# Kernel optimization log

Hardware: AMD Instinct MI355X
Metric: run time of the kernel (lower is better)

The kernel has to match this reference:

```python
import jax, jax.numpy as jnp
import numpy as np

NUM_TASKS, IN_SIZE, OUT_SIZE, N_ROWS = 64, 512, 512, 2048


def setup_inputs() -> dict:
    key = jax.random.key(0)
    k_x, k_t, k_w = jax.random.split(key, 3)
    inputs = jax.random.normal(k_x, (N_ROWS, IN_SIZE), dtype=jnp.float32)
    task_ids = jax.random.randint(k_t, (N_ROWS,), 0, NUM_TASKS, dtype=jnp.int64)
    # in_size == out_size path: identity + N(0, 0.03) perturbation per task
    W = (jnp.eye(IN_SIZE, OUT_SIZE, dtype=jnp.float32)[None]
         + 0.03 * jax.random.normal(k_w, (NUM_TASKS, IN_SIZE, OUT_SIZE), dtype=jnp.float32))
    return {"inputs": inputs, "task_ids": task_ids, "W": W}


def reference(inputs, task_ids, W):
    # Gather the full per-row weight matrix then batched vector-matrix multiply,
    # faithful to torch.einsum('ni,nio->no', inputs, W[task_ids]).
    aligned = W[task_ids]                       # [I, in, out]
    return jnp.einsum("ni,nio->no", inputs, aligned)  # [I, out]
```

## Files before the change

kernel.cpp:

```cpp
#include <hip/hip_runtime.h>


#define NDIM 512
#define KDIM 512
#define NCOL 32
#define KH   256

typedef _Float16 f16x8 __attribute__((ext_vector_type(8)));
typedef float    f32x4 __attribute__((ext_vector_type(4)));
typedef int      i32x4 __attribute__((ext_vector_type(4)));

__global__ __launch_bounds__(256, 4) void k_fused3(
    const float* __restrict__ x,
    const int*   __restrict__ tids,
    const float* __restrict__ W,
    float*       __restrict__ out,
    int n_rows)
{
    const int tid  = threadIdx.x;
    const int lane = tid & 63;
    const int wv   = tid >> 6;

    const int id    = blockIdx.x;
    const int task  = (id & 7) | ((id >> 7) << 3);
    const int c0    = ((id >> 3) & 15) * NCOL;

    __shared__ __align__(16) _Float16 Wt2[2][NCOL * KH];
    __shared__ unsigned short rlw[4 * 128];

    const int rbase = wv * 512 + lane * 8;
    int tval[8];
    if (rbase + 7 < n_rows) {
        const i32x4 a = *(const i32x4*)(tids + rbase);
        const i32x4 b = *(const i32x4*)(tids + rbase + 4);
        tval[0] = a[0]; tval[1] = a[1]; tval[2] = a[2]; tval[3] = a[3];
        tval[4] = b[0]; tval[5] = b[1]; tval[6] = b[2]; tval[7] = b[3];
    } else {
        #pragma unroll
        for (int j = 0; j < 8; ++j)
            tval[j] = (rbase + j < n_rows) ? tids[rbase + j] : -1;
    }

    const int sc4 = (tid & 7) * 4;
    const int ob  = tid >> 3;
    const float* Wg = W + (size_t)task * KDIM * NDIM + c0;
    float4 wr[8];
    #pragma unroll
    for (int j = 0; j < 8; ++j)
        wr[j] = *(const float4*)(Wg + (size_t)(ob * 8 + j) * NDIM + sc4);

    int cloc = 0;
    #pragma unroll
    for (int j = 0; j < 8; ++j) {
        const bool m = (tval[j] == task);
        const unsigned long long bal = __ballot(m);
        const int rank = __popcll(bal & ((1ull << lane) - 1ull));
        if (m) rlw[wv * 128 + cloc + rank] = (unsigned short)(rbase + j);
        cloc += __popcll(bal);
    }

    const int ml = lane & 15;
    const int q  = lane >> 4;

    auto load_half = [&](const float* xr, int t, f16x8* paf) {
        #pragma unroll
        for (int h = 0; h < 2; ++h) {
            f32x4 xa[8];
            #pragma unroll
            for (int k2 = 0; k2 < 4; ++k2) {
                const int ks = h * 4 + k2;
                xa[2 * k2]     = *(const f32x4*)(xr + t * KH + ks * 32 + q * 8);
                xa[2 * k2 + 1] = *(const f32x4*)(xr + t * KH + ks * 32 + q * 8 + 4);
            }
            #pragma unroll
            for (int k2 = 0; k2 < 4; ++k2) {
                f16x8 af;
                const float* a0 = (const float*)&xa[2 * k2];
                #pragma unroll
                for (int j = 0; j < 8; ++j) af[j] = (_Float16)a0[j];
                paf[h * 4 + k2] = af;
            }
        }
    };

    auto stage_half = [&](int t) {
        #pragma unroll
        for (int j2 = 0; j2 < 4; ++j2) {
            f16x8 h8;
            #pragma unroll
            for (int j = 0; j < 8; ++j)
                h8[j] = (_Float16)(((const float*)&wr[j])[j2]);
            const int c  = sc4 + j2;
            const int po = ob ^ (c & 7);
            *(f16x8*)&Wt2[t][c * KH + po * 8] = h8;
        }
    };

    auto mma_half = [&](int t, const f16x8* paf, f32x4* acc) {
        #pragma unroll
        for (int ks = 0; ks < 8; ++ks) {
            #pragma unroll
            for (int ct = 0; ct < 2; ++ct) {
                const int cB = ct * 16 + ml;
                const int po = (ks * 4 + q) ^ (cB & 7);
                const f16x8 bf = *(const f16x8*)&Wt2[t][cB * KH + po * 8];
                acc[ct] = __builtin_amdgcn_mfma_f32_16x16x32_f16(paf[ks], bf, acc[ct], 0, 0, 0);
            }
        }
    };

    auto store_rows = [&](int g0, const f32x4* acc) {
        #pragma unroll
        for (int rg = 0; rg < 4; ++rg) {
            const int pos = g0 + q * 4 + rg;
            if (pos < cloc) {
                float* op = out + (size_t)rlw[wv * 128 + pos] * NDIM + c0 + ml;
                op[0]  = acc[0][rg];
                op[16] = acc[1][rg];
            }
        }
    };

    const float* xr = x;
    f16x8 pafA[8];
    if (cloc > 0) {
        const int idx = (ml < cloc) ? ml : (cloc - 1);
        xr = x + (size_t)rlw[wv * 128 + idx] * KDIM;
        load_half(xr, 0, pafA);
    }

    stage_half(0);
    #pragma unroll
    for (int j = 0; j < 8; ++j)
        wr[j] = *(const float4*)(Wg + (size_t)(KH + ob * 8 + j) * NDIM + sc4);

    asm volatile("s_waitcnt lgkmcnt(0)" ::: "memory");
    __builtin_amdgcn_s_barrier();
    __builtin_amdgcn_sched_barrier(0);

    f32x4 acc[2] = {};
    if (cloc > 0) mma_half(0, pafA, acc);

    f16x8 pafB[8];
    if (cloc > 0) load_half(xr, 1, pafB);

    stage_half(1);

    asm volatile("s_waitcnt lgkmcnt(0)" ::: "memory");
    __builtin_amdgcn_s_barrier();
    __builtin_amdgcn_sched_barrier(0);

    if (cloc > 0) {
        mma_half(1, pafB, acc);
        store_rows(0, acc);
    }

    for (int g0 = 16; g0 < cloc; g0 += 16) {
        const int idx = g0 + ml;
        const float* xr2 = x + (size_t)rlw[wv * 128 + ((idx < cloc) ? idx : (cloc - 1))] * KDIM;
        f16x8 pf[8];
        f32x4 a2[2] = {};
        load_half(xr2, 0, pf);
        mma_half(0, pf, a2);
        load_half(xr2, 1, pf);
        mma_half(1, pf, a2);
        store_rows(g0, a2);
    }
}

extern "C" void kernel_launch(void* const* d_in, const int* in_sizes, int n_in,
                              void* d_out, int out_size, void* d_ws, size_t ws_size,
                              hipStream_t stream) {
    const float* x    = (const float*)d_in[0];
    const int*   tids = (const int*)d_in[1];
    const float* W    = (const float*)d_in[2];
    float*       out  = (float*)d_out;
    const int n_rows  = in_sizes[1];

    k_fused3<<<dim3(1024), dim3(256), 0, stream>>>(x, tids, W, out, n_rows);
}
```

Before: 107.3 us.

## Make blocks persistent over two work units and prefetch next unit's weights

The grid is halved and each block now processes two (task, column-slice) units in sequence. It reuses the loaded task ids and issues the next unit's first weight half while the current unit's MMAs and row tails run. This aims to hide global weight-load latency and amortize block launch and task-id loading. In exchange, per-block parallelism is lower, occupancy hints drop to 2 blocks per CU, and an extra barrier is added between units.

```diff
diff --git a/kernel.cpp b/kernel.cpp
--- a/kernel.cpp
+++ b/kernel.cpp
@@ -5,12 +5,14 @@
 #define KDIM 512
 #define NCOL 32
 #define KH   256
+#define GRID 512
+#define NUNIT 2
 
 typedef _Float16 f16x8 __attribute__((ext_vector_type(8)));
 typedef float    f32x4 __attribute__((ext_vector_type(4)));
 typedef int      i32x4 __attribute__((ext_vector_type(4)));
 
-__global__ __launch_bounds__(256, 4) void k_fused3(
+__global__ __launch_bounds__(256, 2) void k_fused4(
     const float* __restrict__ x,
     const int*   __restrict__ tids,
     const float* __restrict__ W,
@@ -20,12 +22,12 @@
     const int tid  = threadIdx.x;
     const int lane = tid & 63;
     const int wv   = tid >> 6;
-
-    const int id    = blockIdx.x;
-    const int task  = (id & 7) | ((id >> 7) << 3);
-    const int c0    = ((id >> 3) & 15) * NCOL;
-
-    __shared__ __align__(16) _Float16 Wt2[2][NCOL * KH];
+    const int ml   = lane & 15;
+    const int q    = lane >> 4;
+    const int sc4  = (tid & 7) * 4;
+    const int ob   = tid >> 3;
+
+    __shared__ __align__(16) _Float16 Wt[2][NCOL * KH];
     __shared__ unsigned short rlw[4 * 128];
 
     const int rbase = wv * 512 + lane * 8;
@@ -41,36 +43,39 @@
             tval[j] = (rbase + j < n_rows) ? tids[rbase + j] : -1;
     }
 
-    const int sc4 = (tid & 7) * 4;
-    const int ob  = tid >> 3;
-    const float* Wg = W + (size_t)task * KDIM * NDIM + c0;
+    int   cloc = 0;
+    int   c0   = 0;
+    const float* xr = x;
     float4 wr[8];
-    #pragma unroll
-    for (int j = 0; j < 8; ++j)
-        wr[j] = *(const float4*)(Wg + (size_t)(ob * 8 + j) * NDIM + sc4);
-
-    int cloc = 0;
-    #pragma unroll
-    for (int j = 0; j < 8; ++j) {
-        const bool m = (tval[j] == task);
-        const unsigned long long bal = __ballot(m);
-        const int rank = __popcll(bal & ((1ull << lane) - 1ull));
-        if (m) rlw[wv * 128 + cloc + rank] = (unsigned short)(rbase + j);
-        cloc += __popcll(bal);
-    }
-
-    const int ml = lane & 15;
-    const int q  = lane >> 4;
-
-    auto load_half = [&](const float* xr, int t, f16x8* paf) {
+
+    auto issueW = [&](const float* Wg, int h) {
+        #pragma unroll
+        for (int j = 0; j < 8; ++j)
+            wr[j] = *(const float4*)(Wg + (size_t)(h * KH + ob * 8 + j) * NDIM + sc4);
+    };
+
+    auto stageW = [&](int t) {
+        #pragma unroll
+        for (int j2 = 0; j2 < 4; ++j2) {
+            f16x8 h8;
+            #pragma unroll
+            for (int j = 0; j < 8; ++j)
+                h8[j] = (_Float16)(((const float*)&wr[j])[j2]);
+            const int c  = sc4 + j2;
+            const int po = ob ^ (c & 7);
+            *(f16x8*)&Wt[t][c * KH + po * 8] = h8;
+        }
+    };
+
+    auto load_half = [&](const float* xrp, int t, f16x8* paf) {
         #pragma unroll
         for (int h = 0; h < 2; ++h) {
             f32x4 xa[8];
             #pragma unroll
             for (int k2 = 0; k2 < 4; ++k2) {
                 const int ks = h * 4 + k2;
-                xa[2 * k2]     = *(const f32x4*)(xr + t * KH + ks * 32 + q * 8);
-                xa[2 * k2 + 1] = *(const f32x4*)(xr + t * KH + ks * 32 + q * 8 + 4);
+                xa[2 * k2]     = *(const f32x4*)(xrp + t * KH + ks * 32 + q * 8);
+                xa[2 * k2 + 1] = *(const f32x4*)(xrp + t * KH + ks * 32 + q * 8 + 4);
             }
             #pragma unroll
             for (int k2 = 0; k2 < 4; ++k2) {
@@ -83,19 +88,6 @@
         }
     };
 
-    auto stage_half = [&](int t) {
-        #pragma unroll
-        for (int j2 = 0; j2 < 4; ++j2) {
-            f16x8 h8;
-            #pragma unroll
-            for (int j = 0; j < 8; ++j)
-                h8[j] = (_Float16)(((const float*)&wr[j])[j2]);
-            const int c  = sc4 + j2;
-            const int po = ob ^ (c & 7);
-            *(f16x8*)&Wt2[t][c * KH + po * 8] = h8;
-        }
-    };
-
     auto mma_half = [&](int t, const f16x8* paf, f32x4* acc) {
         #pragma unroll
         for (int ks = 0; ks < 8; ++ks) {
@@ -103,7 +95,7 @@
             for (int ct = 0; ct < 2; ++ct) {
                 const int cB = ct * 16 + ml;
                 const int po = (ks * 4 + q) ^ (cB & 7);
-                const f16x8 bf = *(const f16x8*)&Wt2[t][cB * KH + po * 8];
+                const f16x8 bf = *(const f16x8*)&Wt[t][cB * KH + po * 8];
                 acc[ct] = __builtin_amdgcn_mfma_f32_16x16x32_f16(paf[ks], bf, acc[ct], 0, 0, 0);
             }
         }
@@ -121,50 +113,78 @@
         }
     };
 
-    const float* xr = x;
-    f16x8 pafA[8];
-    if (cloc > 0) {
-        const int idx = (ml < cloc) ? ml : (cloc - 1);
-        xr = x + (size_t)rlw[wv * 128 + idx] * KDIM;
-        load_half(xr, 0, pafA);
-    }
-
-    stage_half(0);
+    int task = (blockIdx.x & 7) | ((blockIdx.x >> 7) << 3);
+    c0 = ((blockIdx.x >> 3) & 15) * NCOL;
+    const float* Wg = W + (size_t)task * KDIM * NDIM + c0;
+    issueW(Wg, 0);
+
     #pragma unroll
-    for (int j = 0; j < 8; ++j)
-        wr[j] = *(const float4*)(Wg + (size_t)(KH + ob * 8 + j) * NDIM + sc4);
-
-    asm volatile("s_waitcnt lgkmcnt(0)" ::: "memory");
-    __builtin_amdgcn_s_barrier();
-    __builtin_amdgcn_sched_barrier(0);
-
-    f32x4 acc[2] = {};
-    if (cloc > 0) mma_half(0, pafA, acc);
-
-    f16x8 pafB[8];
-    if (cloc > 0) load_half(xr, 1, pafB);
-
-    stage_half(1);
-
-    asm volatile("s_waitcnt lgkmcnt(0)" ::: "memory");
-    __builtin_amdgcn_s_barrier();
-    __builtin_amdgcn_sched_barrier(0);
-
-    if (cloc > 0) {
-        mma_half(1, pafB, acc);
-        store_rows(0, acc);
-    }
-
-    for (int g0 = 16; g0 < cloc; g0 += 16) {
-        const int idx = g0 + ml;
-        const float* xr2 = x + (size_t)rlw[wv * 128 + ((idx < cloc) ? idx : (cloc - 1))] * KDIM;
-        f16x8 pf[8];
-        f32x4 a2[2] = {};
-        load_half(xr2, 0, pf);
-        mma_half(0, pf, a2);
-        load_half(xr2, 1, pf);
-        mma_half(1, pf, a2);
-        store_rows(g0, a2);
+    for (int uu = 0; uu < NUNIT; ++uu) {
+        cloc = 0;
+        #pragma unroll
+        for (int j = 0; j < 8; ++j) {
+            const bool m = (tval[j] == task);
+            const unsigned long long bal = __ballot(m);
+            const int rank = __popcll(bal & ((1ull << lane) - 1ull));
+            if (m) rlw[wv * 128 + cloc + rank] = (unsigned short)(rbase + j);
+            cloc += __popcll(bal);
+        }
+
+        f16x8 pafA[8], pafB[8];
+        if (cloc > 0) {
+            const int idx = (ml < cloc) ? ml : (cloc - 1);
+            xr = x + (size_t)rlw[wv * 128 + idx] * KDIM;
+            load_half(xr, 0, pafA);
+        }
+
+        stageW(0);
+        issueW(Wg, 1);
+        asm volatile("s_waitcnt lgkmcnt(0)" ::: "memory");
+        __builtin_amdgcn_s_barrier();
+        __builtin_amdgcn_sched_barrier(0);
+
+        f32x4 acc[2] = {};
+        if (cloc > 0) mma_half(0, pafA, acc);
+        if (cloc > 0) load_half(xr, 1, pafB);
+        stageW(1);
+
+        int ntask = 0, nc0 = 0;
+        const float* nWg = nullptr;
+        if (uu + 1 < NUNIT) {
+            const int nu = blockIdx.x + (uu + 1) * GRID;
+            ntask = (nu & 7) | ((nu >> 7) << 3);
+            nc0   = ((nu >> 3) & 15) * NCOL;
+            nWg   = W + (size_t)ntask * KDIM * NDIM + nc0;
+            issueW(nWg, 0);
+        }
+
+        asm volatile("s_waitcnt lgkmcnt(0)" ::: "memory");
+        __builtin_amdgcn_s_barrier();
+        __builtin_amdgcn_sched_barrier(0);
+
+        if (cloc > 0) {
+            mma_half(1, pafB, acc);
+            store_rows(0, acc);
+        }
+
+        for (int g0 = 16; g0 < cloc; g0 += 16) {
+            const int idx = g0 + ml;
+            const float* xr2 = x + (size_t)rlw[wv * 128 + ((idx < cloc) ? idx : (cloc - 1))] * KDIM;
+            f16x8 pf[8];
+            f32x4 a2[2] = {};
+            load_half(xr2, 0, pf);
+            mma_half(0, pf, a2);
+            load_half(xr2, 1, pf);
+            mma_half(1, pf, a2);
+            store_rows(g0, a2);
+        }
+
+        if (uu + 1 < NUNIT) {
+            asm volatile("s_waitcnt lgkmcnt(0)" ::: "memory");
+            __builtin_amdgcn_s_barrier();
+            __builtin_amdgcn_sched_barrier(0);
+            task = ntask; c0 = nc0; Wg = nWg;
+        }
     }
 }
 
@@ -177,5 +197,5 @@
     float*       out  = (float*)d_out;
     const int n_rows  = in_sizes[1];
 
-    k_fused3<<<dim3(1024), dim3(256), 0, stream>>>(x, tids, W, out, n_rows);
+    k_fused4<<<dim3(GRID), dim3(256), 0, stream>>>(x, tids, W, out, n_rows);
 }
```

Result: no change. 105.3 us (-1.8%).

## Widen per-block column tile to 64 and halve grid size

Applied to the files above, without the earlier changes.

Each block now covers 64 output columns instead of 32, so the grid drops from 1024 to 512 blocks. Every routed x row is loaded and converted to fp16 once per 64 columns rather than once per 32, which halves redundant x traffic and conversion work. W staging is split into two register batches with interleaved issue and stage steps to overlap the global loads. The costs are doubled LDS for the weight tile, more registers (launch bounds lowered to 2 blocks per CU), fewer blocks in flight, and a new clamp that caps each wave's row list at 128.

```diff
diff --git a/kernel.cpp b/kernel.cpp
--- a/kernel.cpp
+++ b/kernel.cpp
@@ -3,14 +3,15 @@
 
 #define NDIM 512
 #define KDIM 512
-#define NCOL 32
+#define NCOL 64
 #define KH   256
+#define GRID 512
 
 typedef _Float16 f16x8 __attribute__((ext_vector_type(8)));
 typedef float    f32x4 __attribute__((ext_vector_type(4)));
 typedef int      i32x4 __attribute__((ext_vector_type(4)));
 
-__global__ __launch_bounds__(256, 4) void k_fused3(
+__global__ __launch_bounds__(256, 2) void k_g64(
     const float* __restrict__ x,
     const int*   __restrict__ tids,
     const float* __restrict__ W,
@@ -20,13 +21,20 @@
     const int tid  = threadIdx.x;
     const int lane = tid & 63;
     const int wv   = tid >> 6;
+    const int ml   = lane & 15;
+    const int q    = lane >> 4;
+    const int cg   = tid & 15;
+    const int sc4  = cg * 4;
+    const int ot   = tid >> 4;
 
-    const int id    = blockIdx.x;
-    const int task  = (id & 7) | ((id >> 7) << 3);
-    const int c0    = ((id >> 3) & 15) * NCOL;
+    const int bid   = blockIdx.x;
+    const int task  = (bid & 7) | ((bid >> 6) << 3);
+    const int c0    = ((bid >> 3) & 7) * NCOL;
 
-    __shared__ __align__(16) _Float16 Wt2[2][NCOL * KH];
+    __shared__ __align__(16) _Float16 Wt[2][NCOL * KH];
     __shared__ unsigned short rlw[4 * 128];
+
+    const float* Wg = W + (size_t)task * KDIM * NDIM + c0;
 
     const int rbase = wv * 512 + lane * 8;
     int tval[8];
@@ -41,13 +49,30 @@
             tval[j] = (rbase + j < n_rows) ? tids[rbase + j] : -1;
     }
 
-    const int sc4 = (tid & 7) * 4;
-    const int ob  = tid >> 3;
-    const float* Wg = W + (size_t)task * KDIM * NDIM + c0;
-    float4 wr[8];
-    #pragma unroll
-    for (int j = 0; j < 8; ++j)
-        wr[j] = *(const float4*)(Wg + (size_t)(ob * 8 + j) * NDIM + sc4);
+    float4 wrA[8], wrB[8];
+
+    auto issueS = [&](int h, int s, float4 (&wb)[8]) {
+        const size_t kb = (size_t)(h * KH) + (size_t)(ot + 16 * s) * 8;
+        #pragma unroll
+        for (int j = 0; j < 8; ++j)
+            wb[j] = *(const float4*)(Wg + (kb + j) * NDIM + sc4);
+    };
+    auto stageS = [&](int h, int s, const float4 (&wb)[8]) {
+        const int oct = ot + 16 * s;
+        #pragma unroll
+        for (int j2 = 0; j2 < 4; ++j2) {
+            f16x8 h8;
+            #pragma unroll
+            for (int j = 0; j < 8; ++j)
+                h8[j] = (_Float16)(((const float*)&wb[j])[j2]);
+            const int c  = sc4 + j2;
+            const int po = oct ^ (c & 7);
+            *(f16x8*)&Wt[h][c * KH + po * 8] = h8;
+        }
+    };
+
+    issueS(0, 0, wrA);
+    issueS(0, 1, wrB);
 
     int cloc = 0;
     #pragma unroll
@@ -55,22 +80,21 @@
         const bool m = (tval[j] == task);
         const unsigned long long bal = __ballot(m);
         const int rank = __popcll(bal & ((1ull << lane) - 1ull));
-        if (m) rlw[wv * 128 + cloc + rank] = (unsigned short)(rbase + j);
+        const int slot = cloc + rank;
+        if (m && slot < 128) rlw[wv * 128 + slot] = (unsigned short)(rbase + j);
         cloc += __popcll(bal);
     }
+    if (cloc > 128) cloc = 128;
 
-    const int ml = lane & 15;
-    const int q  = lane >> 4;
-
-    auto load_half = [&](const float* xr, int t, f16x8* paf) {
+    auto load_half = [&](const float* xrp, int t, f16x8* paf) {
         #pragma unroll
         for (int h = 0; h < 2; ++h) {
             f32x4 xa[8];
             #pragma unroll
             for (int k2 = 0; k2 < 4; ++k2) {
                 const int ks = h * 4 + k2;
-                xa[2 * k2]     = *(const f32x4*)(xr + t * KH + ks * 32 + q * 8);
-                xa[2 * k2 + 1] = *(const f32x4*)(xr + t * KH + ks * 32 + q * 8 + 4);
+                xa[2 * k2]     = *(const f32x4*)(xrp + t * KH + ks * 32 + q * 8);
+                xa[2 * k2 + 1] = *(const f32x4*)(xrp + t * KH + ks * 32 + q * 8 + 4);
             }
             #pragma unroll
             for (int k2 = 0; k2 < 4; ++k2) {
@@ -83,27 +107,14 @@
         }
     };
 
-    auto stage_half = [&](int t) {
-        #pragma unroll
-        for (int j2 = 0; j2 < 4; ++j2) {
-            f16x8 h8;
-            #pragma unroll
-            for (int j = 0; j < 8; ++j)
-                h8[j] = (_Float16)(((const float*)&wr[j])[j2]);
-            const int c  = sc4 + j2;
-            const int po = ob ^ (c & 7);
-            *(f16x8*)&Wt2[t][c * KH + po * 8] = h8;
-        }
-    };
-
     auto mma_half = [&](int t, const f16x8* paf, f32x4* acc) {
         #pragma unroll
         for (int ks = 0; ks < 8; ++ks) {
             #pragma unroll
-            for (int ct = 0; ct < 2; ++ct) {
+            for (int ct = 0; ct < 4; ++ct) {
                 const int cB = ct * 16 + ml;
                 const int po = (ks * 4 + q) ^ (cB & 7);
-                const f16x8 bf = *(const f16x8*)&Wt2[t][cB * KH + po * 8];
+                const f16x8 bf = *(const f16x8*)&Wt[t][cB * KH + po * 8];
                 acc[ct] = __builtin_amdgcn_mfma_f32_16x16x32_f16(paf[ks], bf, acc[ct], 0, 0, 0);
             }
         }
@@ -117,34 +128,35 @@
                 float* op = out + (size_t)rlw[wv * 128 + pos] * NDIM + c0 + ml;
                 op[0]  = acc[0][rg];
                 op[16] = acc[1][rg];
+                op[32] = acc[2][rg];
+                op[48] = acc[3][rg];
             }
         }
     };
 
     const float* xr = x;
-    f16x8 pafA[8];
+    f16x8 pafA[8], pafB[8];
     if (cloc > 0) {
         const int idx = (ml < cloc) ? ml : (cloc - 1);
         xr = x + (size_t)rlw[wv * 128 + idx] * KDIM;
         load_half(xr, 0, pafA);
     }
 
-    stage_half(0);
-    #pragma unroll
-    for (int j = 0; j < 8; ++j)
-        wr[j] = *(const float4*)(Wg + (size_t)(KH + ob * 8 + j) * NDIM + sc4);
+    stageS(0, 0, wrA);
+    issueS(1, 0, wrA);
+    stageS(0, 1, wrB);
+    issueS(1, 1, wrB);
 
     asm volatile("s_waitcnt lgkmcnt(0)" ::: "memory");
     __builtin_amdgcn_s_barrier();
     __builtin_amdgcn_sched_barrier(0);
 
-    f32x4 acc[2] = {};
+    f32x4 acc[4] = {};
     if (cloc > 0) mma_half(0, pafA, acc);
-
-    f16x8 pafB[8];
     if (cloc > 0) load_half(xr, 1, pafB);
 
-    stage_half(1);
+    stageS(1, 0, wrA);
+    stageS(1, 1, wrB);
 
     asm volatile("s_waitcnt lgkmcnt(0)" ::: "memory");
     __builtin_amdgcn_s_barrier();
@@ -159,7 +171,7 @@
         const int idx = g0 + ml;
         const float* xr2 = x + (size_t)rlw[wv * 128 + ((idx < cloc) ? idx : (cloc - 1))] * KDIM;
         f16x8 pf[8];
-        f32x4 a2[2] = {};
+        f32x4 a2[4] = {};
         load_half(xr2, 0, pf);
         mma_half(0, pf, a2);
         load_half(xr2, 1, pf);
@@ -177,5 +189,5 @@
     float*       out  = (float*)d_out;
     const int n_rows  = in_sizes[1];
 
-    k_fused3<<<dim3(1024), dim3(256), 0, stream>>>(x, tids, W, out, n_rows);
+    k_g64<<<dim3(GRID), dim3(256), 0, stream>>>(x, tids, W, out, n_rows);
 }
```

New measurement: 103.7 us (median of 2 runs). -3.3%, faster.
